# Kernel optimization log

Measured on AMD Instinct MI355X. Metric: run time of the kernel, lower is better.

The kernel has to match this reference:

```python
import jax, jax.numpy as jnp
import numpy as np

B, C_IN, H, W = 8, 32, 64, 64
C = 64  # num_channels


def setup_inputs() -> dict:
    key = jax.random.key(0)
    ks = jax.random.split(key, 9)
    s_in = 1.0 / np.sqrt(C_IN)
    s_c = 1.0 / np.sqrt(C)
    return {
        "x": jax.random.normal(ks[0], (B, C_IN, H, W), dtype=jnp.float32),
        "wq": jax.random.uniform(ks[1], (C, C_IN), jnp.float32, -s_in, s_in),
        "bq": jax.random.uniform(ks[2], (C,), jnp.float32, -s_in, s_in),
        "wk": jax.random.uniform(ks[3], (C, C_IN), jnp.float32, -s_in, s_in),
        "bk": jax.random.uniform(ks[4], (C,), jnp.float32, -s_in, s_in),
        "wv": jax.random.uniform(ks[5], (C, C_IN), jnp.float32, -s_in, s_in),
        "bv": jax.random.uniform(ks[6], (C,), jnp.float32, -s_in, s_in),
        "wo": jax.random.uniform(ks[7], (C_IN, C), jnp.float32, -s_c, s_c),
        "bo": jax.random.uniform(ks[8], (C_IN,), jnp.float32, -s_c, s_c),
    }


def reference(x, wq, bq, wk, bk, wv, bv, wo, bo):
    b, c_in, h, w = x.shape
    n = h * w
    # 1x1 convs == per-pixel linear projections; produce (B, N, C) directly
    q = (jnp.einsum('bchw,oc->bhwo', x, wq) + bq).reshape(b, n, -1)
    k = (jnp.einsum('bchw,oc->bhwo', x, wk) + bk).reshape(b, n, -1)
    v = (jnp.einsum('bchw,oc->bhwo', x, wv) + bv).reshape(b, n, -1)
    # unscaled attention over spatial positions (no 1/sqrt(d) in original)
    scores = jnp.einsum('bnc,bmc->bnm', q, k)  # (B, N, N)
    attn = jax.nn.softmax(scores, axis=-1)
    out = jnp.einsum('bnm,bmc->bnc', attn, v)  # (B, N, C)
    out = out.reshape(b, h, w, -1)
    out = jnp.einsum('bhwc,oc->bohw', out, wo) + bo[None, :, None, None]
    return out + x
```

## Files before the change

kernel.cpp:

```cpp
#include <hip/hip_runtime.h>
#include <hip/hip_bf16.h>

#define CIN    32
#define NPIX   4096
#define DIM    64
#define LOG2E  1.4426950408889634f

#if __has_builtin(__builtin_amdgcn_exp2f)
#define EXP2(x) __builtin_amdgcn_exp2f(x)
#else
#define EXP2(x) exp2f(x)
#endif

typedef float  f32x4 __attribute__((ext_vector_type(4)));
typedef short  s16x8 __attribute__((ext_vector_type(8)));
typedef short  s16x4 __attribute__((ext_vector_type(4)));

__device__ __forceinline__ f32x4 mfma16(s16x4 a, s16x4 b, f32x4 c) {
#if __has_builtin(__builtin_amdgcn_mfma_f32_16x16x16bf16_1k)
    return __builtin_amdgcn_mfma_f32_16x16x16bf16_1k(a, b, c, 0, 0, 0);
#elif __has_builtin(__builtin_amdgcn_mfma_f32_16x16x16_bf16)
    return __builtin_amdgcn_mfma_f32_16x16x16_bf16(a, b, c, 0, 0, 0);
#else
    f32x4 d;
    asm("v_mfma_f32_16x16x16_bf16 %0, %1, %2, %3" : "=v"(d) : "v"(a), "v"(b), "v"(c));
    return d;
#endif
}


__global__ __launch_bounds__(256) void qkv_proj(
    const float* __restrict__ x,
    const float* __restrict__ wq, const float* __restrict__ bq,
    const float* __restrict__ wk, const float* __restrict__ bk,
    const float* __restrict__ wv, const float* __restrict__ bv,
    __hip_bfloat16* __restrict__ qb, __hip_bfloat16* __restrict__ kb,
    __hip_bfloat16* __restrict__ vb)
{
    __shared__ float Xs[CIN][64];
    __shared__ float wT[3][CIN][DIM];

    const int tid = threadIdx.x;
    const int b   = blockIdx.y;
    const int bx  = blockIdx.x;
    const int n0  = bx * 64;

    for (int i = tid; i < 3 * CIN * DIM; i += 256) {
        int m = i >> 11, r = i & 2047, c = r >> 6, o = r & 63;
        const float* wsrc = (m == 0) ? wq : (m == 1) ? wk : wv;
        float wv0 = wsrc[o * CIN + c];
        wT[m][c][o] = (m == 0) ? wv0 * LOG2E : wv0;
    }
    for (int i = tid * 4; i < CIN * 64; i += 1024) {
        int c = i >> 6, p = i & 63;
        *(f32x4*)&Xs[c][p] = *(const f32x4*)&x[((size_t)b * CIN + c) * NPIX + n0 + p];
    }
    __syncthreads();

    const int w    = tid >> 6;
    const int lane = tid & 63;
    const int l16  = lane >> 2;
    const int quad = lane & 3;

    const int T  = bx * 4 + w;
    const int px = T * 16 + l16;

    float aq[2][8], ak[2][8];
    #pragma unroll
    for (int kb2 = 0; kb2 < 2; kb2++) {
        f32x4 bq0 = *(const f32x4*)&bq[kb2 * 32 + quad * 8];
        f32x4 bq1 = *(const f32x4*)&bq[kb2 * 32 + quad * 8 + 4];
        f32x4 bk0 = *(const f32x4*)&bk[kb2 * 32 + quad * 8];
        f32x4 bk1 = *(const f32x4*)&bk[kb2 * 32 + quad * 8 + 4];
        #pragma unroll
        for (int j = 0; j < 4; j++) {
            aq[kb2][j] = bq0[j] * LOG2E; aq[kb2][j + 4] = bq1[j] * LOG2E;
            ak[kb2][j] = bk0[j];         ak[kb2][j + 4] = bk1[j];
        }
    }
    #pragma unroll 8
    for (int c = 0; c < CIN; c++) {
        const float xc = Xs[c][w * 16 + l16];
        #pragma unroll
        for (int kb2 = 0; kb2 < 2; kb2++) {
            f32x4 q0 = *(const f32x4*)&wT[0][c][kb2 * 32 + quad * 8];
            f32x4 q1 = *(const f32x4*)&wT[0][c][kb2 * 32 + quad * 8 + 4];
            f32x4 k0 = *(const f32x4*)&wT[1][c][kb2 * 32 + quad * 8];
            f32x4 k1 = *(const f32x4*)&wT[1][c][kb2 * 32 + quad * 8 + 4];
            #pragma unroll
            for (int j = 0; j < 4; j++) {
                aq[kb2][j]     += xc * q0[j];
                aq[kb2][j + 4] += xc * q1[j];
                ak[kb2][j]     += xc * k0[j];
                ak[kb2][j + 4] += xc * k1[j];
            }
        }
    }
    #pragma unroll
    for (int kb2 = 0; kb2 < 2; kb2++) {
        union { s16x8 v; __hip_bfloat16 h[8]; } pq, pk;
        #pragma unroll
        for (int j = 0; j < 8; j++) {
            pq.h[j] = __float2bfloat16(aq[kb2][j]);
            pk.h[j] = __float2bfloat16(ak[kb2][j]);
        }
        *(s16x8*)(qb + ((size_t)b * NPIX + px) * DIM + kb2 * 32 + quad * 8) = pq.v;
        const size_t koff =
            ((((size_t)(b * 256 + T) * 2 + kb2) * 16 + l16) * 4 + quad) * 8;
        *(s16x8*)(kb + koff) = pk.v;
    }

    const int ch = w * 16 + l16;
    float av[2][8];
    {
        const float bvc = bv[ch];
        #pragma unroll
        for (int kh = 0; kh < 2; kh++)
            #pragma unroll
            for (int j = 0; j < 8; j++) av[kh][j] = bvc;
    }
    #pragma unroll 8
    for (int c = 0; c < CIN; c++) {
        const float wvc = wT[2][c][ch];
        f32x4 x0 = *(const f32x4*)&Xs[c][quad * 8];
        f32x4 x1 = *(const f32x4*)&Xs[c][quad * 8 + 4];
        f32x4 x2 = *(const f32x4*)&Xs[c][32 + quad * 8];
        f32x4 x3 = *(const f32x4*)&Xs[c][32 + quad * 8 + 4];
        #pragma unroll
        for (int j = 0; j < 4; j++) {
            av[0][j]     += x0[j] * wvc;
            av[0][j + 4] += x1[j] * wvc;
            av[1][j]     += x2[j] * wvc;
            av[1][j + 4] += x3[j] * wvc;
        }
    }
    #pragma unroll
    for (int kh = 0; kh < 2; kh++) {
        #pragma unroll
        for (int h = 0; h < 2; h++) {
            union { unsigned long long u; __hip_bfloat16 hh[4]; } pv;
            #pragma unroll
            for (int j = 0; j < 4; j++) pv.hh[j] = __float2bfloat16(av[kh][h * 4 + j]);
            const int lanep = ((quad & 1) * 2 + h) * 16 + l16;
            const size_t chunk =
                (((size_t)(b * 128 + bx * 2 + kh) * 4 + w) * 64 + lanep) * 2 + (quad >> 1);
            *(unsigned long long*)(vb + chunk * 4) = pv.u;
        }
    }
}

__global__ __launch_bounds__(256, 2) void attn_fused(
    const __hip_bfloat16* __restrict__ qb,
    const __hip_bfloat16* __restrict__ kbf,
    const __hip_bfloat16* __restrict__ vbf,
    const float* __restrict__ wo, const float* __restrict__ bo,
    const float* __restrict__ x, float* __restrict__ y)
{
    __shared__ __align__(16) float RED[3][64][66];
    __shared__ float LRED[3][64];

    const int tid  = threadIdx.x;
    const int kq   = tid >> 6;
    const int lane = tid & 63;
    const int quad = lane >> 4, l16 = lane & 15;
    const int b    = blockIdx.x;
    const int row0 = blockIdx.y * 64;

    s16x8 qf[4][2];
    #pragma unroll
    for (int mt = 0; mt < 4; mt++)
        #pragma unroll
        for (int kb2 = 0; kb2 < 2; kb2++)
            qf[mt][kb2] = *(const s16x8*)(qb
                + ((size_t)b * NPIX + row0 + mt * 16 + l16) * DIM + kb2 * 32 + quad * 8);

    const f32x4 zero4 = {0.f, 0.f, 0.f, 0.f};
    f32x4 o[4][4];
    #pragma unroll
    for (int mt = 0; mt < 4; mt++)
        #pragma unroll
        for (int ct = 0; ct < 4; ct++) o[mt][ct] = zero4;
    f32x4 ol[4] = {zero4, zero4, zero4, zero4};

    s16x4 ones;
    #pragma unroll
    for (int j = 0; j < 4; j++) ones[j] = (short)0x3F80;

    const char* kp = (const char*)kbf + (size_t)b * 524288 + kq * 131072
                     + (l16 * 4 + quad) * 16;
    const char* vp = (const char*)vbf + (size_t)b * 524288 + kq * 131072
                     + lane * 16;

    s16x8 ckA[4], cvA[4], ckB[4], cvB[4];
    #pragma unroll
    for (int i = 0; i < 4; i++) {
        ckA[i] = *(const s16x8*)(kp + i * 1024);
        cvA[i] = *(const s16x8*)(vp + i * 1024);
    }

    auto step = [&](s16x8 (&curK)[4], s16x8 (&curV)[4],
                    s16x8 (&nxtK)[4], s16x8 (&nxtV)[4]) {
        kp += 4096; vp += 4096;
        f32x4 st[2][4];
        #pragma unroll
        for (int nt = 0; nt < 2; nt++)
            #pragma unroll
            for (int mt = 0; mt < 4; mt++) {
                st[nt][mt] = __builtin_amdgcn_mfma_f32_16x16x32_bf16(
                    curK[nt * 2 + 0], qf[mt][0], zero4, 0, 0, 0);
                st[nt][mt] = __builtin_amdgcn_mfma_f32_16x16x32_bf16(
                    curK[nt * 2 + 1], qf[mt][1], st[nt][mt], 0, 0, 0);
            }
        #pragma unroll
        for (int i = 0; i < 4; i++) nxtK[i] = *(const s16x8*)(kp + i * 1024);

        s16x4 pb[2][4];
        #pragma unroll
        for (int nt = 0; nt < 2; nt++)
            #pragma unroll
            for (int mt = 0; mt < 4; mt++) {
                f32x4 p = st[nt][mt];
                #pragma unroll
                for (int r = 0; r < 4; r++) p[r] = EXP2(p[r]);
                union { unsigned int d[2]; s16x4 v; } pk;
                pk.d[0] = (__float_as_uint(p[1]) & 0xffff0000u)
                        | (__float_as_uint(p[0]) >> 16);
                pk.d[1] = (__float_as_uint(p[3]) & 0xffff0000u)
                        | (__float_as_uint(p[2]) >> 16);
                pb[nt][mt] = pk.v;
            }

        #pragma unroll
        for (int ct = 0; ct < 4; ct++) {
            s16x4 vlo = __builtin_shufflevector(curV[ct], curV[ct], 0, 1, 2, 3);
            s16x4 vhi = __builtin_shufflevector(curV[ct], curV[ct], 4, 5, 6, 7);
            #pragma unroll
            for (int mt = 0; mt < 4; mt++) {
                o[mt][ct] = mfma16(vlo, pb[0][mt], o[mt][ct]);
                o[mt][ct] = mfma16(vhi, pb[1][mt], o[mt][ct]);
            }
        }
        #pragma unroll
        for (int mt = 0; mt < 4; mt++) {
            ol[mt] = mfma16(ones, pb[0][mt], ol[mt]);
            ol[mt] = mfma16(ones, pb[1][mt], ol[mt]);
        }
        #pragma unroll
        for (int i = 0; i < 4; i++) nxtV[i] = *(const s16x8*)(vp + i * 1024);
    };

    for (int it = 0; it < 16; it++) {
        step(ckA, cvA, ckB, cvB);
        step(ckB, cvB, ckA, cvA);
    }

    if (kq != 0) {
        #pragma unroll
        for (int mt = 0; mt < 4; mt++) {
            #pragma unroll
            for (int ct = 0; ct < 4; ct++)
                #pragma unroll
                for (int r = 0; r < 4; r++)
                    RED[kq - 1][ct * 16 + quad * 4 + r][mt * 16 + l16] = o[mt][ct][r];
            if (quad == 0)
                LRED[kq - 1][mt * 16 + l16] = ol[mt][0];
        }
    }
    __syncthreads();

    if (kq == 0) {
        #pragma unroll
        for (int reg = 0; reg < 3; reg++)
            #pragma unroll
            for (int mt = 0; mt < 4; mt++) {
                ol[mt][0] += LRED[reg][mt * 16 + l16];
                #pragma unroll
                for (int ct = 0; ct < 4; ct++)
                    #pragma unroll
                    for (int r = 0; r < 4; r++)
                        o[mt][ct][r] += RED[reg][ct * 16 + quad * 4 + r][mt * 16 + l16];
            }

        s16x4 pvo[4][4];
        #pragma unroll
        for (int mt = 0; mt < 4; mt++) {
            const float inv = 1.0f / ol[mt][0];
            #pragma unroll
            for (int ct = 0; ct < 4; ct++) {
                union { s16x4 v; __hip_bfloat16 h[4]; } pk;
                #pragma unroll
                for (int r = 0; r < 4; r++)
                    pk.h[r] = __float2bfloat16(o[mt][ct][r] * inv);
                pvo[mt][ct] = pk.v;
            }
        }

        s16x4 aw[2][4];
        #pragma unroll
        for (int nt = 0; nt < 2; nt++)
            #pragma unroll
            for (int ct = 0; ct < 4; ct++) {
                f32x4 w4 = *(const f32x4*)(wo + (size_t)(nt * 16 + l16) * DIM
                                           + ct * 16 + quad * 4);
                union { s16x4 v; __hip_bfloat16 h[4]; } wf;
                #pragma unroll
                for (int j = 0; j < 4; j++) wf.h[j] = __float2bfloat16(w4[j]);
                aw[nt][ct] = wf.v;
            }

        f32x4 d2[4][2];
        #pragma unroll
        for (int mt = 0; mt < 4; mt++)
            #pragma unroll
            for (int nt = 0; nt < 2; nt++) d2[mt][nt] = zero4;
        #pragma unroll
        for (int ct = 0; ct < 4; ct++)
            #pragma unroll
            for (int nt = 0; nt < 2; nt++)
                #pragma unroll
                for (int mt = 0; mt < 4; mt++)
                    d2[mt][nt] = mfma16(aw[nt][ct], pvo[mt][ct], d2[mt][nt]);

        #pragma unroll
        for (int nt = 0; nt < 2; nt++)
            #pragma unroll
            for (int r = 0; r < 4; r++) {
                const int out = nt * 16 + quad * 4 + r;
                const float bias = bo[out];
                #pragma unroll
                for (int mt = 0; mt < 4; mt++) {
                    const int row = row0 + mt * 16 + l16;
                    const size_t xi = ((size_t)b * CIN + out) * NPIX + row;
                    y[xi] = d2[mt][nt][r] + bias + x[xi];
                }
            }
    }
}

extern "C" void kernel_launch(void* const* d_in, const int* in_sizes, int n_in,
                              void* d_out, int out_size, void* d_ws, size_t ws_size,
                              hipStream_t stream)
{
    const float* x  = (const float*)d_in[0];
    const float* wq = (const float*)d_in[1];
    const float* bq = (const float*)d_in[2];
    const float* wk = (const float*)d_in[3];
    const float* bk = (const float*)d_in[4];
    const float* wv = (const float*)d_in[5];
    const float* bv = (const float*)d_in[6];
    const float* wo = (const float*)d_in[7];
    const float* bo = (const float*)d_in[8];
    float* y = (float*)d_out;

    char* ws = (char*)d_ws;
    __hip_bfloat16* qb = (__hip_bfloat16*)(ws);
    __hip_bfloat16* kb = (__hip_bfloat16*)(ws + (4u << 20));
    __hip_bfloat16* vb = (__hip_bfloat16*)(ws + (8u << 20));

    qkv_proj<<<dim3(64, 8), dim3(256), 0, stream>>>(x, wq, bq, wk, bk, wv, bv, qb, kb, vb);
    attn_fused<<<dim3(8, 64), dim3(256), 0, stream>>>(qb, kb, vb, wo, bo, x, y);
}
```

Before: 132.2 us.

## Halve query rows per block, raise occupancy, distribute epilogue across all waves

Each block now handles 32 query rows instead of 64, which doubles the grid to 1024 blocks and shrinks the per-wave accumulator state so launch bounds can ask for 4 blocks per SIMD group. The double-buffered K/V register ping-pong is replaced by a single set of registers that is reloaded in place. The cross-wave reduction and output projection are now split so all four waves each finish one 16x16 tile, instead of wave 0 doing all of it. The intent is better latency hiding through occupancy and a more balanced epilogue. The cost is that each K/V tile is read by twice as many blocks, and the load-to-use distance inside a wave is shorter.

```diff
diff --git a/kernel.cpp b/kernel.cpp
--- a/kernel.cpp
+++ b/kernel.cpp
@@ -149,38 +149,38 @@
     }
 }
 
-__global__ __launch_bounds__(256, 2) void attn_fused(
+__global__ __launch_bounds__(256, 4) void attn_fused(
     const __hip_bfloat16* __restrict__ qb,
     const __hip_bfloat16* __restrict__ kbf,
     const __hip_bfloat16* __restrict__ vbf,
     const float* __restrict__ wo, const float* __restrict__ bo,
     const float* __restrict__ x, float* __restrict__ y)
 {
-    __shared__ __align__(16) float RED[3][64][66];
-    __shared__ float LRED[3][64];
+    __shared__ __align__(16) float RED[4][2][64][18];
+    __shared__ float LRED[4][2][16];
 
     const int tid  = threadIdx.x;
     const int kq   = tid >> 6;
     const int lane = tid & 63;
     const int quad = lane >> 4, l16 = lane & 15;
     const int b    = blockIdx.x;
-    const int row0 = blockIdx.y * 64;
-
-    s16x8 qf[4][2];
-    #pragma unroll
-    for (int mt = 0; mt < 4; mt++)
+    const int row0 = blockIdx.y * 32;
+
+    s16x8 qf[2][2];
+    #pragma unroll
+    for (int mt = 0; mt < 2; mt++)
         #pragma unroll
         for (int kb2 = 0; kb2 < 2; kb2++)
             qf[mt][kb2] = *(const s16x8*)(qb
                 + ((size_t)b * NPIX + row0 + mt * 16 + l16) * DIM + kb2 * 32 + quad * 8);
 
     const f32x4 zero4 = {0.f, 0.f, 0.f, 0.f};
-    f32x4 o[4][4];
-    #pragma unroll
-    for (int mt = 0; mt < 4; mt++)
+    f32x4 o[2][4];
+    #pragma unroll
+    for (int mt = 0; mt < 2; mt++)
         #pragma unroll
         for (int ct = 0; ct < 4; ct++) o[mt][ct] = zero4;
-    f32x4 ol[4] = {zero4, zero4, zero4, zero4};
+    f32x4 ol[2] = {zero4, zero4};
 
     s16x4 ones;
     #pragma unroll
@@ -191,34 +191,33 @@
     const char* vp = (const char*)vbf + (size_t)b * 524288 + kq * 131072
                      + lane * 16;
 
-    s16x8 ckA[4], cvA[4], ckB[4], cvB[4];
+    s16x8 ck[4], cv[4];
     #pragma unroll
     for (int i = 0; i < 4; i++) {
-        ckA[i] = *(const s16x8*)(kp + i * 1024);
-        cvA[i] = *(const s16x8*)(vp + i * 1024);
-    }
-
-    auto step = [&](s16x8 (&curK)[4], s16x8 (&curV)[4],
-                    s16x8 (&nxtK)[4], s16x8 (&nxtV)[4]) {
+        ck[i] = *(const s16x8*)(kp + i * 1024);
+        cv[i] = *(const s16x8*)(vp + i * 1024);
+    }
+
+    for (int t = 0; t < 32; ++t) {
         kp += 4096; vp += 4096;
-        f32x4 st[2][4];
+        f32x4 st[2][2];
         #pragma unroll
         for (int nt = 0; nt < 2; nt++)
             #pragma unroll
-            for (int mt = 0; mt < 4; mt++) {
+            for (int mt = 0; mt < 2; mt++) {
                 st[nt][mt] = __builtin_amdgcn_mfma_f32_16x16x32_bf16(
-                    curK[nt * 2 + 0], qf[mt][0], zero4, 0, 0, 0);
+                    ck[nt * 2 + 0], qf[mt][0], zero4, 0, 0, 0);
                 st[nt][mt] = __builtin_amdgcn_mfma_f32_16x16x32_bf16(
-                    curK[nt * 2 + 1], qf[mt][1], st[nt][mt], 0, 0, 0);
+                    ck[nt * 2 + 1], qf[mt][1], st[nt][mt], 0, 0, 0);
             }
         #pragma unroll
-        for (int i = 0; i < 4; i++) nxtK[i] = *(const s16x8*)(kp + i * 1024);
-
-        s16x4 pb[2][4];
+        for (int i = 0; i < 4; i++) ck[i] = *(const s16x8*)(kp + i * 1024);
+
+        s16x4 pb[2][2];
         #pragma unroll
         for (int nt = 0; nt < 2; nt++)
             #pragma unroll
-            for (int mt = 0; mt < 4; mt++) {
+            for (int mt = 0; mt < 2; mt++) {
                 f32x4 p = st[nt][mt];
                 #pragma unroll
                 for (int r = 0; r < 4; r++) p[r] = EXP2(p[r]);
@@ -232,108 +231,84 @@
 
         #pragma unroll
         for (int ct = 0; ct < 4; ct++) {
-            s16x4 vlo = __builtin_shufflevector(curV[ct], curV[ct], 0, 1, 2, 3);
-            s16x4 vhi = __builtin_shufflevector(curV[ct], curV[ct], 4, 5, 6, 7);
-            #pragma unroll
-            for (int mt = 0; mt < 4; mt++) {
+            s16x4 vlo = __builtin_shufflevector(cv[ct], cv[ct], 0, 1, 2, 3);
+            s16x4 vhi = __builtin_shufflevector(cv[ct], cv[ct], 4, 5, 6, 7);
+            #pragma unroll
+            for (int mt = 0; mt < 2; mt++) {
                 o[mt][ct] = mfma16(vlo, pb[0][mt], o[mt][ct]);
                 o[mt][ct] = mfma16(vhi, pb[1][mt], o[mt][ct]);
             }
         }
         #pragma unroll
-        for (int mt = 0; mt < 4; mt++) {
+        for (int mt = 0; mt < 2; mt++) {
             ol[mt] = mfma16(ones, pb[0][mt], ol[mt]);
             ol[mt] = mfma16(ones, pb[1][mt], ol[mt]);
         }
         #pragma unroll
-        for (int i = 0; i < 4; i++) nxtV[i] = *(const s16x8*)(vp + i * 1024);
-    };
-
-    for (int it = 0; it < 16; it++) {
-        step(ckA, cvA, ckB, cvB);
-        step(ckB, cvB, ckA, cvA);
-    }
-
-    if (kq != 0) {
-        #pragma unroll
-        for (int mt = 0; mt < 4; mt++) {
-            #pragma unroll
-            for (int ct = 0; ct < 4; ct++)
-                #pragma unroll
-                for (int r = 0; r < 4; r++)
-                    RED[kq - 1][ct * 16 + quad * 4 + r][mt * 16 + l16] = o[mt][ct][r];
-            if (quad == 0)
-                LRED[kq - 1][mt * 16 + l16] = ol[mt][0];
-        }
+        for (int i = 0; i < 4; i++) cv[i] = *(const s16x8*)(vp + i * 1024);
+    }
+
+    #pragma unroll
+    for (int mt = 0; mt < 2; mt++) {
+        #pragma unroll
+        for (int ct = 0; ct < 4; ct++)
+            #pragma unroll
+            for (int r = 0; r < 4; r++)
+                RED[kq][mt][ct * 16 + quad * 4 + r][l16] = o[mt][ct][r];
+        if (quad == 0) LRED[kq][mt][l16] = ol[mt][0];
     }
     __syncthreads();
 
-    if (kq == 0) {
-        #pragma unroll
-        for (int reg = 0; reg < 3; reg++)
-            #pragma unroll
-            for (int mt = 0; mt < 4; mt++) {
-                ol[mt][0] += LRED[reg][mt * 16 + l16];
-                #pragma unroll
-                for (int ct = 0; ct < 4; ct++)
-                    #pragma unroll
-                    for (int r = 0; r < 4; r++)
-                        o[mt][ct][r] += RED[reg][ct * 16 + quad * 4 + r][mt * 16 + l16];
-            }
-
-        s16x4 pvo[4][4];
-        #pragma unroll
-        for (int mt = 0; mt < 4; mt++) {
-            const float inv = 1.0f / ol[mt][0];
-            #pragma unroll
-            for (int ct = 0; ct < 4; ct++) {
-                union { s16x4 v; __hip_bfloat16 h[4]; } pk;
-                #pragma unroll
-                for (int r = 0; r < 4; r++)
-                    pk.h[r] = __float2bfloat16(o[mt][ct][r] * inv);
-                pvo[mt][ct] = pk.v;
-            }
-        }
-
-        s16x4 aw[2][4];
-        #pragma unroll
-        for (int nt = 0; nt < 2; nt++)
-            #pragma unroll
-            for (int ct = 0; ct < 4; ct++) {
-                f32x4 w4 = *(const f32x4*)(wo + (size_t)(nt * 16 + l16) * DIM
-                                           + ct * 16 + quad * 4);
-                union { s16x4 v; __hip_bfloat16 h[4]; } wf;
-                #pragma unroll
-                for (int j = 0; j < 4; j++) wf.h[j] = __float2bfloat16(w4[j]);
-                aw[nt][ct] = wf.v;
-            }
-
-        f32x4 d2[4][2];
-        #pragma unroll
-        for (int mt = 0; mt < 4; mt++)
-            #pragma unroll
-            for (int nt = 0; nt < 2; nt++) d2[mt][nt] = zero4;
+    const int emt = kq >> 1, ent = kq & 1;
+    float osum[4][4];
+    float lsum = 0.f;
+    #pragma unroll
+    for (int ct = 0; ct < 4; ct++)
+        #pragma unroll
+        for (int r = 0; r < 4; r++) osum[ct][r] = 0.f;
+    #pragma unroll
+    for (int k2 = 0; k2 < 4; k2++) {
+        lsum += LRED[k2][emt][l16];
         #pragma unroll
         for (int ct = 0; ct < 4; ct++)
             #pragma unroll
-            for (int nt = 0; nt < 2; nt++)
-                #pragma unroll
-                for (int mt = 0; mt < 4; mt++)
-                    d2[mt][nt] = mfma16(aw[nt][ct], pvo[mt][ct], d2[mt][nt]);
-
-        #pragma unroll
-        for (int nt = 0; nt < 2; nt++)
-            #pragma unroll
-            for (int r = 0; r < 4; r++) {
-                const int out = nt * 16 + quad * 4 + r;
-                const float bias = bo[out];
-                #pragma unroll
-                for (int mt = 0; mt < 4; mt++) {
-                    const int row = row0 + mt * 16 + l16;
-                    const size_t xi = ((size_t)b * CIN + out) * NPIX + row;
-                    y[xi] = d2[mt][nt][r] + bias + x[xi];
-                }
-            }
+            for (int r = 0; r < 4; r++)
+                osum[ct][r] += RED[k2][emt][ct * 16 + quad * 4 + r][l16];
+    }
+
+    const float inv = 1.0f / lsum;
+    s16x4 pvo[4];
+    #pragma unroll
+    for (int ct = 0; ct < 4; ct++) {
+        union { s16x4 v; __hip_bfloat16 h[4]; } pk;
+        #pragma unroll
+        for (int r = 0; r < 4; r++)
+            pk.h[r] = __float2bfloat16(osum[ct][r] * inv);
+        pvo[ct] = pk.v;
+    }
+
+    s16x4 aw[4];
+    #pragma unroll
+    for (int ct = 0; ct < 4; ct++) {
+        f32x4 w4 = *(const f32x4*)(wo + (size_t)(ent * 16 + l16) * DIM
+                                   + ct * 16 + quad * 4);
+        union { s16x4 v; __hip_bfloat16 h[4]; } wf;
+        #pragma unroll
+        for (int j = 0; j < 4; j++) wf.h[j] = __float2bfloat16(w4[j]);
+        aw[ct] = wf.v;
+    }
+
+    f32x4 d2 = zero4;
+    #pragma unroll
+    for (int ct = 0; ct < 4; ct++)
+        d2 = mfma16(aw[ct], pvo[ct], d2);
+
+    #pragma unroll
+    for (int r = 0; r < 4; r++) {
+        const int out = ent * 16 + quad * 4 + r;
+        const int row = row0 + emt * 16 + l16;
+        const size_t xi = ((size_t)b * CIN + out) * NPIX + row;
+        y[xi] = d2[r] + bo[out] + x[xi];
     }
 }
 
@@ -358,5 +333,5 @@
     __hip_bfloat16* vb = (__hip_bfloat16*)(ws + (8u << 20));
 
     qkv_proj<<<dim3(64, 8), dim3(256), 0, stream>>>(x, wq, bq, wk, bk, wv, bv, qb, kb, vb);
-    attn_fused<<<dim3(8, 64), dim3(256), 0, stream>>>(qb, kb, vb, wo, bo, x, y);
+    attn_fused<<<dim3(8, 128), dim3(256), 0, stream>>>(qb, kb, vb, wo, bo, x, y);
 }
```

After: 137.7 us. 1.04x slower.

## Split attention key range across eight waves with tree reduction

Applied to the files above, without the earlier changes.

Doubles the attention block to 512 threads. Each of eight waves handles half as many key/value tiles as before, and the per-wave partial outputs are combined with a three-stage LDS tree reduction instead of one wave summing three partials. The P-to-bf16 packing now uses rounding conversions instead of bit truncation. The aim is more latency hiding and shorter per-wave loops, but the launch bounds of (512,4) may cap registers hard enough to cause spills, the larger shared buffer limits resident blocks, and the rounding adds ALU work in the inner loop.

```diff
diff --git a/kernel.cpp b/kernel.cpp
--- a/kernel.cpp
+++ b/kernel.cpp
@@ -149,15 +149,15 @@
     }
 }
 
-__global__ __launch_bounds__(256, 2) void attn_fused(
+__global__ __launch_bounds__(512, 4) void attn_fused(
     const __hip_bfloat16* __restrict__ qb,
     const __hip_bfloat16* __restrict__ kbf,
     const __hip_bfloat16* __restrict__ vbf,
     const float* __restrict__ wo, const float* __restrict__ bo,
     const float* __restrict__ x, float* __restrict__ y)
 {
-    __shared__ __align__(16) float RED[3][64][66];
-    __shared__ float LRED[3][64];
+    __shared__ __align__(16) float RED[4][64][66];
+    __shared__ float LRED[4][64];
 
     const int tid  = threadIdx.x;
     const int kq   = tid >> 6;
@@ -186,9 +186,9 @@
     #pragma unroll
     for (int j = 0; j < 4; j++) ones[j] = (short)0x3F80;
 
-    const char* kp = (const char*)kbf + (size_t)b * 524288 + kq * 131072
+    const char* kp = (const char*)kbf + (size_t)b * 524288 + kq * 65536
                      + (l16 * 4 + quad) * 16;
-    const char* vp = (const char*)vbf + (size_t)b * 524288 + kq * 131072
+    const char* vp = (const char*)vbf + (size_t)b * 524288 + kq * 65536
                      + lane * 16;
 
     s16x8 ckA[4], cvA[4], ckB[4], cvB[4];
@@ -222,11 +222,9 @@
                 f32x4 p = st[nt][mt];
                 #pragma unroll
                 for (int r = 0; r < 4; r++) p[r] = EXP2(p[r]);
-                union { unsigned int d[2]; s16x4 v; } pk;
-                pk.d[0] = (__float_as_uint(p[1]) & 0xffff0000u)
-                        | (__float_as_uint(p[0]) >> 16);
-                pk.d[1] = (__float_as_uint(p[3]) & 0xffff0000u)
-                        | (__float_as_uint(p[2]) >> 16);
+                union { s16x4 v; __hip_bfloat16 h[4]; } pk;
+                #pragma unroll
+                for (int r = 0; r < 4; r++) pk.h[r] = __float2bfloat16(p[r]);
                 pb[nt][mt] = pk.v;
             }
 
@@ -249,37 +247,80 @@
         for (int i = 0; i < 4; i++) nxtV[i] = *(const s16x8*)(vp + i * 1024);
     };
 
-    for (int it = 0; it < 16; it++) {
+    for (int it = 0; it < 8; it++) {
         step(ckA, cvA, ckB, cvB);
         step(ckB, cvB, ckA, cvA);
     }
 
-    if (kq != 0) {
-        #pragma unroll
-        for (int mt = 0; mt < 4; mt++) {
-            #pragma unroll
-            for (int ct = 0; ct < 4; ct++)
-                #pragma unroll
-                for (int r = 0; r < 4; r++)
-                    RED[kq - 1][ct * 16 + quad * 4 + r][mt * 16 + l16] = o[mt][ct][r];
-            if (quad == 0)
-                LRED[kq - 1][mt * 16 + l16] = ol[mt][0];
+    if (kq >= 4) {
+        #pragma unroll
+        for (int mt = 0; mt < 4; mt++) {
+            #pragma unroll
+            for (int ct = 0; ct < 4; ct++)
+                #pragma unroll
+                for (int r = 0; r < 4; r++)
+                    RED[kq - 4][ct * 16 + quad * 4 + r][mt * 16 + l16] = o[mt][ct][r];
+            if (quad == 0) LRED[kq - 4][mt * 16 + l16] = ol[mt][0];
         }
     }
     __syncthreads();
+    if (kq < 4) {
+        #pragma unroll
+        for (int mt = 0; mt < 4; mt++) {
+            ol[mt][0] += LRED[kq][mt * 16 + l16];
+            #pragma unroll
+            for (int ct = 0; ct < 4; ct++)
+                #pragma unroll
+                for (int r = 0; r < 4; r++)
+                    o[mt][ct][r] += RED[kq][ct * 16 + quad * 4 + r][mt * 16 + l16];
+        }
+    }
+    if (kq == 2 || kq == 3) {
+        #pragma unroll
+        for (int mt = 0; mt < 4; mt++) {
+            #pragma unroll
+            for (int ct = 0; ct < 4; ct++)
+                #pragma unroll
+                for (int r = 0; r < 4; r++)
+                    RED[kq][ct * 16 + quad * 4 + r][mt * 16 + l16] = o[mt][ct][r];
+            if (quad == 0) LRED[kq][mt * 16 + l16] = ol[mt][0];
+        }
+    }
+    __syncthreads();
+    if (kq < 2) {
+        #pragma unroll
+        for (int mt = 0; mt < 4; mt++) {
+            ol[mt][0] += LRED[kq + 2][mt * 16 + l16];
+            #pragma unroll
+            for (int ct = 0; ct < 4; ct++)
+                #pragma unroll
+                for (int r = 0; r < 4; r++)
+                    o[mt][ct][r] += RED[kq + 2][ct * 16 + quad * 4 + r][mt * 16 + l16];
+        }
+    }
+    if (kq == 1) {
+        #pragma unroll
+        for (int mt = 0; mt < 4; mt++) {
+            #pragma unroll
+            for (int ct = 0; ct < 4; ct++)
+                #pragma unroll
+                for (int r = 0; r < 4; r++)
+                    RED[1][ct * 16 + quad * 4 + r][mt * 16 + l16] = o[mt][ct][r];
+            if (quad == 0) LRED[1][mt * 16 + l16] = ol[mt][0];
+        }
+    }
+    __syncthreads();
 
     if (kq == 0) {
         #pragma unroll
-        for (int reg = 0; reg < 3; reg++)
-            #pragma unroll
-            for (int mt = 0; mt < 4; mt++) {
-                ol[mt][0] += LRED[reg][mt * 16 + l16];
-                #pragma unroll
-                for (int ct = 0; ct < 4; ct++)
-                    #pragma unroll
-                    for (int r = 0; r < 4; r++)
-                        o[mt][ct][r] += RED[reg][ct * 16 + quad * 4 + r][mt * 16 + l16];
-            }
+        for (int mt = 0; mt < 4; mt++) {
+            ol[mt][0] += LRED[1][mt * 16 + l16];
+            #pragma unroll
+            for (int ct = 0; ct < 4; ct++)
+                #pragma unroll
+                for (int r = 0; r < 4; r++)
+                    o[mt][ct][r] += RED[1][ct * 16 + quad * 4 + r][mt * 16 + l16];
+        }
 
         s16x4 pvo[4][4];
         #pragma unroll
@@ -358,5 +399,5 @@
     __hip_bfloat16* vb = (__hip_bfloat16*)(ws + (8u << 20));
 
     qkv_proj<<<dim3(64, 8), dim3(256), 0, stream>>>(x, wq, bq, wk, bk, wv, bv, qb, kb, vb);
-    attn_fused<<<dim3(8, 64), dim3(256), 0, stream>>>(qb, kb, vb, wo, bo, x, y);
+    attn_fused<<<dim3(8, 64), dim3(512), 0, stream>>>(qb, kb, vb, wo, bo, x, y);
 }
```

After: 404.7 us. 206% more time.
